# Kernel optimization log

Hardware: AMD Instinct MI355X
Metric: run time of the kernel (lower is better)

The kernel has to match this reference:

```python
import jax, jax.numpy as jnp
import numpy as np

EMB = 512   # emb_dim (== hsz, required by init_decoder feeding enc_sum as hidden)
HSZ = 512   # decoder hidden size
KW, BSZ, PLY = 24, 64, 32  # kw_num, batch, ply_num (decode length = PLY)


def setup_inputs() -> dict:
    key = jax.random.key(0)
    ks = jax.random.split(key, 16)
    s = np.float32(1.0 / np.sqrt(HSZ))
    return {
        "home_col_rep": jax.random.normal(ks[0], (KW, BSZ, PLY, EMB), jnp.float32),
        "home_indices": jax.random.randint(ks[1], (BSZ * KW, PLY), 0, PLY, dtype=jnp.int64),
        "vis_col_rep": jax.random.normal(ks[2], (KW, BSZ, PLY, EMB), jnp.float32),
        "vis_indices": jax.random.randint(ks[3], (BSZ * KW, PLY), 0, PLY, dtype=jnp.int64),
        "team_col_rep": jax.random.normal(ks[4], (KW, BSZ, PLY, EMB), jnp.float32),
        "team_indices": jax.random.randint(ks[5], (BSZ * KW, PLY), 0, PLY, dtype=jnp.int64),
        # learned params
        "init_embed": jax.random.uniform(ks[6], (EMB,), jnp.float32, -1.0, 1.0),
        "W_ih": jax.random.normal(ks[7], (4 * HSZ, EMB), jnp.float32) * s,
        "W_hh": jax.random.normal(ks[8], (4 * HSZ, HSZ), jnp.float32) * s,
        "b_ih": jax.random.normal(ks[9], (4 * HSZ,), jnp.float32) * s,
        "b_hh": jax.random.normal(ks[10], (4 * HSZ,), jnp.float32) * s,
        "Wq": jax.random.normal(ks[11], (HSZ, HSZ), jnp.float32) * s,
        "bq": jax.random.normal(ks[12], (HSZ,), jnp.float32) * s,
        "Wc": jax.random.normal(ks[13], (HSZ, EMB), jnp.float32) * s,
        "v": jax.random.normal(ks[14], (HSZ,), jnp.float32) * s,
    }


def _once(enc4, idx, init_embed, W_ih, W_hh, b_ih, b_hh, Wq, bq, Wc, v):
    kw, bsz, ply, h = enc4.shape
    B = bsz * kw
    # sort_type='col': (kw,bsz,ply,h) -> (bsz,kw,ply,h) -> (B,ply,h)
    enc = jnp.transpose(enc4, (1, 0, 2, 3)).reshape(B, ply, h)
    # gather decoder inputs by indices
    dec_in = jnp.take_along_axis(enc, idx[:, :, None], axis=1)  # (B,ply,h)
    # tgt = [init_embed, dec_in][:-1] -> ply steps
    steps = jnp.concatenate(
        [jnp.broadcast_to(init_embed, (B, 1, h)), dec_in[:, :-1]], axis=1
    )  # (B,ply,h)
    h0 = enc.sum(axis=1)  # (B,h) -> both h and c init (LSTM)
    ctx = jnp.einsum("bpe,he->bph", enc, Wc)  # linear_context, precomputed

    def step(carry, x_t):
        hh, cc = carry
        gates = x_t @ W_ih.T + b_ih + hh @ W_hh.T + b_hh  # (B,4h)
        i, f, g, o = jnp.split(gates, 4, axis=-1)
        cc = jax.nn.sigmoid(f) * cc + jax.nn.sigmoid(i) * jnp.tanh(g)
        hh = jax.nn.sigmoid(o) * jnp.tanh(cc)
        q = hh @ Wq.T + bq                      # linear_query
        sc = jnp.tanh(q[:, None, :] + ctx) @ v  # (B,ply)
        logp = jax.nn.log_softmax(sc, axis=-1)
        return (hh, cc), (logp, jnp.argmax(logp, axis=-1))

    (_, _), (attns, argmaxs) = jax.lax.scan(step, (h0, h0), jnp.transpose(steps, (1, 0, 2)))
    # attns: (ply,B,ply) -> (B,ply,ply); argmaxs: (ply,B) -> (B,ply,1)
    return jnp.transpose(attns, (1, 0, 2)), jnp.transpose(argmaxs)[..., None]


def reference(home_col_rep, home_indices, vis_col_rep, vis_indices,
              team_col_rep, team_indices, init_embed, W_ih, W_hh, b_ih, b_hh,
              Wq, bq, Wc, v):
    p = (init_embed, W_ih, W_hh, b_ih, b_hh, Wq, bq, Wc, v)
    h_att, h_arg = _once(home_col_rep, home_indices, *p)
    v_att, v_arg = _once(vis_col_rep, vis_indices, *p)
    t_att, t_arg = _once(team_col_rep, team_indices, *p)
    return (h_att, v_att, t_att, h_arg, v_arg, t_arg)
```

## Files before the change

### kernel.cpp

```cpp
#include <hip/hip_runtime.h>
#include <hip/hip_bf16.h>
#include <math.h>

#define KW 24
#define BSZn 64
#define PLY 32
#define BROWS 1536
#define RTOT 4608

typedef __attribute__((ext_vector_type(8))) short short8v;
typedef __attribute__((ext_vector_type(4))) float f32x4;

__device__ __forceinline__ float sigmoidf_(float x) { return 1.0f / (1.0f + expf(-x)); }

__device__ __forceinline__ float tanh_fast(float x)
{
    float xc = fminf(fmaxf(x, -40.0f), 40.0f);
    float t = __expf(2.0f * xc);
    return (t - 1.0f) * __builtin_amdgcn_rcpf(t + 1.0f);
}

__device__ __forceinline__ void gload16(const void* g, void* l)
{
    __builtin_amdgcn_global_load_lds(
        (__attribute__((address_space(1))) void*)g,
        (__attribute__((address_space(3))) void*)l, 16, 0, 0);
}

__device__ __forceinline__ void split3(float v, ushort* a, ushort* b, ushort* c)
{
    __hip_bfloat16 h1 = __float2bfloat16(v);  float f1 = __bfloat162float(h1);
    float r1 = v - f1;
    __hip_bfloat16 h2 = __float2bfloat16(r1); float f2 = __bfloat162float(h2);
    float r2 = r1 - f2;
    __hip_bfloat16 h3 = __float2bfloat16(r2);
    *a = *(ushort*)&h1; *b = *(ushort*)&h2; *c = *(ushort*)&h3;
}

__global__ void prep_split(const float* __restrict__ W_ih, const float* __restrict__ W_hh,
                           const float* __restrict__ Wq, const float* __restrict__ Wc,
                           const float* __restrict__ b_ih, const float* __restrict__ b_hh,
                           ushort* __restrict__ Wg0, ushort* __restrict__ Wg1, ushort* __restrict__ Wg2,
                           ushort* __restrict__ Wq0, ushort* __restrict__ Wq1, ushort* __restrict__ Wq2,
                           ushort* __restrict__ Wc0, ushort* __restrict__ Wc1, ushort* __restrict__ Wc2,
                           float* __restrict__ biasG)
{
    int n = blockIdx.x, tid = threadIdx.x;
    if (n < 2048) {
        int ublk = n >> 6, gate = (n >> 4) & 3, ui = n & 15;
        int src = gate * 512 + ublk * 16 + ui;
        for (int k = tid; k < 1024; k += 256) {
            float v = (k < 512) ? W_ih[(size_t)src * 512 + k]
                                : W_hh[(size_t)src * 512 + (k - 512)];
            ushort s0, s1, s2; split3(v, &s0, &s1, &s2);
            Wg0[(size_t)n * 1024 + k] = s0;
            Wg1[(size_t)n * 1024 + k] = s1;
            Wg2[(size_t)n * 1024 + k] = s2;
        }
        if (tid == 0) biasG[src] = b_ih[src] + b_hh[src];
    } else if (n < 2560) {
        int n2 = n - 2048;
        for (int k = tid; k < 512; k += 256) {
            ushort s0, s1, s2; split3(Wq[(size_t)n2 * 512 + k], &s0, &s1, &s2);
            Wq0[(size_t)n2 * 512 + k] = s0;
            Wq1[(size_t)n2 * 512 + k] = s1;
            Wq2[(size_t)n2 * 512 + k] = s2;
        }
    } else {
        int n2 = n - 2560;
        for (int k = tid; k < 512; k += 256) {
            ushort s0, s1, s2; split3(Wc[(size_t)n2 * 512 + k], &s0, &s1, &s2);
            Wc0[(size_t)n2 * 512 + k] = s0;
            Wc1[(size_t)n2 * 512 + k] = s1;
            Wc2[(size_t)n2 * 512 + k] = s2;
        }
    }
}

__global__ void init0(const float* __restrict__ home, const float* __restrict__ vis,
                      const float* __restrict__ team,
                      float* __restrict__ cst, float* __restrict__ hf0)
{
    int row = blockIdx.x, tid = threadIdx.x;
    int tau = row / BROWS, r = row % BROWS;
    const float* enc = (tau == 0) ? home : (tau == 1) ? vis : team;
    const float* base = enc + ((size_t)((r % KW) * BSZn + r / KW) * PLY) * 512;
    for (int e = tid; e < 512; e += 256) {
        float s = 0.0f;
        for (int p = 0; p < PLY; ++p) s += base[(size_t)p * 512 + e];
        size_t o = (size_t)row * 512 + e;
        cst[o] = s;
        hf0[o] = s;
    }
}

__global__ __launch_bounds__(256) void gates_mfma(
    const float* __restrict__ home, const float* __restrict__ vis, const float* __restrict__ team,
    const int* __restrict__ hidx, const int* __restrict__ vidx, const int* __restrict__ tidx,
    const float* __restrict__ init_embed,
    const float* __restrict__ hf_in,
    const ushort* __restrict__ Wg0, const ushort* __restrict__ Wg1, const ushort* __restrict__ Wg2,
    const ushort* __restrict__ Wq0, const ushort* __restrict__ Wq1, const ushort* __restrict__ Wq2,
    const float* __restrict__ biasG, const float* __restrict__ bq,
    float* __restrict__ cst, float* __restrict__ hf_out,
    float* __restrict__ Q4, int bn_off, int qslot, int t)
{
    __shared__ char Lds[49152];
    int tid = threadIdx.x;
    int bm = blockIdx.x, bn = blockIdx.y + bn_off;
    bool isq = bn >= 16;
    int w = tid >> 6, lane = tid & 63;
    int wr = w >> 1, wc = w & 1;
    int r0 = bm * 128;
    int nbase = isq ? (bn - 16) * 128 : bn * 128;
    int ldb = isq ? 512 : 1024;
    int kb0 = isq ? 16 : 0;
    int l4 = lane >> 2, lc = lane & 3;
    int srow = tid >> 1, sh = tid & 1;

    const float* hrow = hf_in + (size_t)(r0 + srow) * 512;
    const float* xrow = init_embed;
    if (!isq && t > 0) {
        int tau = (bm * 128) / BROWS;
        const float* enc = (tau == 0) ? home : (tau == 1) ? vis : team;
        const int* idx = (tau == 0) ? hidx : (tau == 1) ? vidx : tidx;
        int r = r0 + srow - tau * BROWS;
        int j = idx[r * PLY + (t - 1)];
        xrow = enc + ((size_t)((r % KW) * BSZn + r / KW) * PLY + j) * 512;
    }
    const ushort* Bp[3];
    if (isq) { Bp[0] = Wq0; Bp[1] = Wq1; Bp[2] = Wq2; }
    else     { Bp[0] = Wg0; Bp[1] = Wg1; Bp[2] = Wg2; }

    f32x4 acc[4][4];
    #pragma unroll
    for (int i = 0; i < 4; ++i)
        #pragma unroll
        for (int j = 0; j < 4; ++j) acc[i][j] = (f32x4){0.f, 0.f, 0.f, 0.f};

    char* ldsBw = Lds + 24576 + w * 2048;
    char* aw = Lds + srow * 64 + sh * 32;

    for (int kb = kb0; kb < 32; ++kb) {
        int kloc = (kb & 15) * 32;
        const float* src = (!isq && kb < 16) ? xrow : hrow;
        float fv[16];
        *(float4*)&fv[0]  = *(const float4*)(src + kloc + sh * 16);
        *(float4*)&fv[4]  = *(const float4*)(src + kloc + sh * 16 + 4);
        *(float4*)&fv[8]  = *(const float4*)(src + kloc + sh * 16 + 8);
        *(float4*)&fv[12] = *(const float4*)(src + kloc + sh * 16 + 12);
        int bofe = isq ? kloc : kb * 32;
        __syncthreads();
        #pragma unroll
        for (int p = 0; p < 3; ++p) {
            gload16(Bp[p] + (size_t)(nbase + w * 32 + l4) * ldb + bofe + lc * 8,
                    ldsBw + p * 8192);
            gload16(Bp[p] + (size_t)(nbase + w * 32 + 16 + l4) * ldb + bofe + lc * 8,
                    ldsBw + p * 8192 + 1024);
        }
        union { ushort u[16]; uint4 v[2]; } u0, u1, u2;
        #pragma unroll
        for (int j2 = 0; j2 < 16; ++j2) split3(fv[j2], &u0.u[j2], &u1.u[j2], &u2.u[j2]);
        *(uint4*)(aw)              = u0.v[0];
        *(uint4*)(aw + 16)         = u0.v[1];
        *(uint4*)(aw + 8192)       = u1.v[0];
        *(uint4*)(aw + 8192 + 16)  = u1.v[1];
        *(uint4*)(aw + 16384)      = u2.v[0];
        *(uint4*)(aw + 16384 + 16) = u2.v[1];
        __syncthreads();

        #pragma unroll
        for (int a = 0; a < 3; ++a) {
            short8v af[4];
            #pragma unroll
            for (int fm = 0; fm < 4; ++fm)
                af[fm] = *(const short8v*)(Lds + a * 8192 +
                           (wr * 64 + fm * 16 + (lane & 15)) * 64 + (lane >> 4) * 16);
            #pragma unroll
            for (int b = 2; b >= 0; --b) {
                if (a + b > 2) continue;
                const char* LdsB = Lds + 24576 + b * 8192;
                short8v bf[4];
                #pragma unroll
                for (int fn = 0; fn < 4; ++fn)
                    bf[fn] = *(const short8v*)(LdsB +
                               (wc * 64 + fn * 16 + (lane & 15)) * 64 + (lane >> 4) * 16);
                #pragma unroll
                for (int fm = 0; fm < 4; ++fm)
                    #pragma unroll
                    for (int fn = 0; fn < 4; ++fn)
                        acc[fm][fn] = __builtin_amdgcn_mfma_f32_16x16x32_bf16(
                            af[fm], bf[fn], acc[fm][fn], 0, 0, 0);
            }
        }
    }

    if (!isq) {
        int u = (bn * 2 + wc) * 16 + (lane & 15);
        float bI = biasG[u], bF = biasG[512 + u], bG = biasG[1024 + u], bO = biasG[1536 + u];
        #pragma unroll
        for (int fm = 0; fm < 4; ++fm) {
            #pragma unroll
            for (int reg = 0; reg < 4; ++reg) {
                int row = r0 + wr * 64 + fm * 16 + (lane >> 4) * 4 + reg;
                float gi = acc[fm][0][reg] + bI;
                float gf = acc[fm][1][reg] + bF;
                float gg = acc[fm][2][reg] + bG;
                float go = acc[fm][3][reg] + bO;
                size_t ci = (size_t)row * 512 + u;
                float c = cst[ci];
                c = sigmoidf_(gf) * c + sigmoidf_(gi) * tanhf(gg);
                float h = sigmoidf_(go) * tanhf(c);
                cst[ci] = c;
                hf_out[ci] = h;
            }
        }
    } else {
        float* Qout = Q4 + (size_t)qslot * RTOT * 512;
        #pragma unroll
        for (int fn = 0; fn < 4; ++fn) {
            int col = nbase + wc * 64 + fn * 16 + (lane & 15);
            float bqv = bq[col];
            #pragma unroll
            for (int fm = 0; fm < 4; ++fm)
                #pragma unroll
                for (int reg = 0; reg < 4; ++reg) {
                    int row = r0 + wr * 64 + fm * 16 + (lane >> 4) * 4 + reg;
                    Qout[(size_t)row * 512 + col] = acc[fm][fn][reg] + bqv;
                }
        }
    }
}

__global__ __launch_bounds__(256) void ctx_mfma(
    const float* __restrict__ home, const float* __restrict__ vis, const float* __restrict__ team,
    const ushort* __restrict__ Wc0, const ushort* __restrict__ Wc1, const ushort* __restrict__ Wc2,
    float* __restrict__ ctx)
{
    __shared__ char Lds[49152];
    int tid = threadIdx.x;
    int bm = blockIdx.x, bn = blockIdx.y;
    int w = tid >> 6, lane = tid & 63;
    int wr = w >> 1, wc = w & 1;
    int r0 = bm * 128;
    int nbase = bn * 128;
    int l4 = lane >> 2, lc = lane & 3;
    int srow = tid >> 1, sh = tid & 1;

    int R = r0 + srow;
    int tau = r0 / (BROWS * PLY);
    const float* enc = (tau == 0) ? home : (tau == 1) ? vis : team;
    int rr = R % (BROWS * PLY), r = rr >> 5, p = rr & 31;
    const float* arow = enc + ((size_t)((r % KW) * BSZn + r / KW) * PLY + p) * 512;
    const ushort* Bp[3] = {Wc0, Wc1, Wc2};

    f32x4 acc[4][4];
    #pragma unroll
    for (int i = 0; i < 4; ++i)
        #pragma unroll
        for (int j = 0; j < 4; ++j) acc[i][j] = (f32x4){0.f, 0.f, 0.f, 0.f};

    char* ldsBw = Lds + 24576 + w * 2048;
    char* aw = Lds + srow * 64 + sh * 32;

    for (int kb = 0; kb < 16; ++kb) {
        int kloc = kb * 32;
        float fv[16];
        *(float4*)&fv[0]  = *(const float4*)(arow + kloc + sh * 16);
        *(float4*)&fv[4]  = *(const float4*)(arow + kloc + sh * 16 + 4);
        *(float4*)&fv[8]  = *(const float4*)(arow + kloc + sh * 16 + 8);
        *(float4*)&fv[12] = *(const float4*)(arow + kloc + sh * 16 + 12);
        __syncthreads();
        #pragma unroll
        for (int pp = 0; pp < 3; ++pp) {
            gload16(Bp[pp] + (size_t)(nbase + w * 32 + l4) * 512 + kloc + lc * 8,
                    ldsBw + pp * 8192);
            gload16(Bp[pp] + (size_t)(nbase + w * 32 + 16 + l4) * 512 + kloc + lc * 8,
                    ldsBw + pp * 8192 + 1024);
        }
        union { ushort u[16]; uint4 v[2]; } u0, u1, u2;
        #pragma unroll
        for (int j2 = 0; j2 < 16; ++j2) split3(fv[j2], &u0.u[j2], &u1.u[j2], &u2.u[j2]);
        *(uint4*)(aw)              = u0.v[0];
        *(uint4*)(aw + 16)         = u0.v[1];
        *(uint4*)(aw + 8192)       = u1.v[0];
        *(uint4*)(aw + 8192 + 16)  = u1.v[1];
        *(uint4*)(aw + 16384)      = u2.v[0];
        *(uint4*)(aw + 16384 + 16) = u2.v[1];
        __syncthreads();

        #pragma unroll
        for (int a = 0; a < 3; ++a) {
            short8v af[4];
            #pragma unroll
            for (int fm = 0; fm < 4; ++fm)
                af[fm] = *(const short8v*)(Lds + a * 8192 +
                           (wr * 64 + fm * 16 + (lane & 15)) * 64 + (lane >> 4) * 16);
            #pragma unroll
            for (int b = 2; b >= 0; --b) {
                if (a + b > 2) continue;
                const char* LdsB = Lds + 24576 + b * 8192;
                short8v bf[4];
                #pragma unroll
                for (int fn = 0; fn < 4; ++fn)
                    bf[fn] = *(const short8v*)(LdsB +
                               (wc * 64 + fn * 16 + (lane & 15)) * 64 + (lane >> 4) * 16);
                #pragma unroll
                for (int fm = 0; fm < 4; ++fm)
                    #pragma unroll
                    for (int fn = 0; fn < 4; ++fn)
                        acc[fm][fn] = __builtin_amdgcn_mfma_f32_16x16x32_bf16(
                            af[fm], bf[fn], acc[fm][fn], 0, 0, 0);
            }
        }
    }

    #pragma unroll
    for (int fn = 0; fn < 4; ++fn) {
        int col = nbase + wc * 64 + fn * 16 + (lane & 15);
        #pragma unroll
        for (int fm = 0; fm < 4; ++fm)
            #pragma unroll
            for (int reg = 0; reg < 4; ++reg) {
                int row = r0 + wr * 64 + fm * 16 + (lane >> 4) * 4 + reg;
                ctx[(size_t)row * 512 + col] = acc[fm][fn][reg];
            }
    }
}

__global__ __launch_bounds__(256) void attn4r(
    const float* __restrict__ Q4, const float* __restrict__ ctx,
    const float* __restrict__ vvec, float* __restrict__ out, int tbase)
{
    int row = blockIdx.x, tid = threadIdx.x;
    int w = tid >> 6, lane = tid & 63;
    __shared__ float scs[4][PLY];

    float qv[4][8], vv[8];
    #pragma unroll
    for (int s = 0; s < 4; ++s) {
        const float* q = Q4 + ((size_t)s * RTOT + row) * 512 + lane * 8;
        *(float4*)&qv[s][0] = *(const float4*)(q);
        *(float4*)&qv[s][4] = *(const float4*)(q + 4);
    }
    *(float4*)&vv[0] = *(const float4*)(vvec + lane * 8);
    *(float4*)&vv[4] = *(const float4*)(vvec + lane * 8 + 4);
    const float* ctxr = ctx + (size_t)row * PLY * 512 + lane * 8;

    for (int pp = 0; pp < 8; ++pp) {
        int p = w * 8 + pp;
        const float* cp = ctxr + (size_t)p * 512;
        float cv[8];
        *(float4*)&cv[0] = *(const float4*)(cp);
        *(float4*)&cv[4] = *(const float4*)(cp + 4);
        float a[4] = {0.f, 0.f, 0.f, 0.f};
        #pragma unroll
        for (int j = 0; j < 8; ++j) {
            float c = cv[j], ve = vv[j];
            #pragma unroll
            for (int s = 0; s < 4; ++s)
                a[s] += tanh_fast(qv[s][j] + c) * ve;
        }
        #pragma unroll
        for (int off = 1; off < 64; off <<= 1) {
            #pragma unroll
            for (int s = 0; s < 4; ++s) a[s] += __shfl_xor(a[s], off);
        }
        if (lane == 0) {
            #pragma unroll
            for (int s = 0; s < 4; ++s) scs[s][p] = a[s];
        }
    }
    __syncthreads();

    if (tid < 128) {
        int w2 = tid >> 5, l = tid & 31;
        float x = scs[w2][l];
        float bvv = x; int bi = l;
        #pragma unroll
        for (int off = 1; off < 32; off <<= 1) {
            float ov = __shfl_xor(bvv, off, 32);
            int oi = __shfl_xor(bi, off, 32);
            if (ov > bvv || (ov == bvv && oi < bi)) { bvv = ov; bi = oi; }
        }
        float s = expf(x - bvv);
        #pragma unroll
        for (int off = 1; off < 32; off <<= 1) s += __shfl_xor(s, off, 32);
        float lse = logf(s);
        int t = tbase + w2;
        int tau = row / BROWS, r = row % BROWS;
        out[(size_t)tau * (BROWS * 1024) + (size_t)r * 1024 + t * 32 + l] = x - bvv - lse;
        if (l == 0)
            out[(size_t)3 * (BROWS * 1024) + (size_t)tau * (BROWS * 32) + r * 32 + t] = (float)bi;
    }
}

extern "C" void kernel_launch(void* const* d_in, const int* in_sizes, int n_in,
                              void* d_out, int out_size, void* d_ws, size_t ws_size,
                              hipStream_t stream)
{
    const float* home = (const float*)d_in[0];
    const int*   hidx = (const int*)d_in[1];
    const float* vis  = (const float*)d_in[2];
    const int*   vidx = (const int*)d_in[3];
    const float* team = (const float*)d_in[4];
    const int*   tidx = (const int*)d_in[5];
    const float* init_embed = (const float*)d_in[6];
    const float* W_ih = (const float*)d_in[7];
    const float* W_hh = (const float*)d_in[8];
    const float* b_ih = (const float*)d_in[9];
    const float* b_hh = (const float*)d_in[10];
    const float* Wq   = (const float*)d_in[11];
    const float* bq   = (const float*)d_in[12];
    const float* Wc   = (const float*)d_in[13];
    const float* vvec = (const float*)d_in[14];
    float* out = (float*)d_out;
    (void)in_sizes; (void)n_in; (void)out_size; (void)ws_size;

    char* wsb = (char*)d_ws;
    float* ctx   = (float*)wsb; wsb += (size_t)RTOT * PLY * 512 * 4;
    float* cst   = (float*)wsb; wsb += (size_t)RTOT * 512 * 4;
    float* Q4    = (float*)wsb; wsb += (size_t)4 * RTOT * 512 * 4;
    float* biasG = (float*)wsb; wsb += 2048 * 4;
    ushort* Wg[3], *Wq3[3], *Wc3[3];
    for (int i = 0; i < 3; ++i) { Wg[i]  = (ushort*)wsb; wsb += (size_t)2048 * 1024 * 2; }
    for (int i = 0; i < 3; ++i) { Wq3[i] = (ushort*)wsb; wsb += (size_t)512 * 512 * 2; }
    for (int i = 0; i < 3; ++i) { Wc3[i] = (ushort*)wsb; wsb += (size_t)512 * 512 * 2; }
    float* hf[2];
    for (int b = 0; b < 2; ++b) { hf[b] = (float*)wsb; wsb += (size_t)RTOT * 512 * 4; }

    prep_split<<<3072, 256, 0, stream>>>(W_ih, W_hh, Wq, Wc, b_ih, b_hh,
                                         Wg[0], Wg[1], Wg[2], Wq3[0], Wq3[1], Wq3[2],
                                         Wc3[0], Wc3[1], Wc3[2], biasG);
    init0<<<RTOT, 256, 0, stream>>>(home, vis, team, cst, hf[1]);
    ctx_mfma<<<dim3(RTOT * PLY / 128, 4), 256, 0, stream>>>(
        home, vis, team, Wc3[0], Wc3[1], Wc3[2], ctx);

    for (int t = 0; t < 32; ++t) {
        int hin = (t + 1) & 1, hout = t & 1;
        int gy = 16 + ((t >= 1) ? 4 : 0);
        gates_mfma<<<dim3(36, gy), 256, 0, stream>>>(
            home, vis, team, hidx, vidx, tidx, init_embed,
            hf[hin],
            Wg[0], Wg[1], Wg[2], Wq3[0], Wq3[1], Wq3[2],
            biasG, bq, cst, hf[hout],
            Q4, 0, (t - 1) & 3, t);
        if (t >= 4 && (t & 3) == 0)
            attn4r<<<RTOT, 256, 0, stream>>>(Q4, ctx, vvec, out, t - 4);
    }
    gates_mfma<<<dim3(36, 4), 256, 0, stream>>>(
        home, vis, team, hidx, vidx, tidx, init_embed,
        hf[1],
        Wg[0], Wg[1], Wg[2], Wq3[0], Wq3[1], Wq3[2],
        biasG, bq, cst, hf[0],
        Q4, 16, 3, 32);
    attn4r<<<RTOT, 256, 0, stream>>>(Q4, ctx, vvec, out, 28);
}
```

Measured before the change: 6.445 ms.

## Widen gates GEMM N-tile to 256 columns to halve A-tile reloads

The per-step gates/query GEMM kernel now computes a 128x256 output tile per block instead of 128x128. Each wave holds 4x8 accumulators, and the LDS B buffer is doubled, so shared memory grows to 72KB. The goal is to halve redundant loading and bf16 splitting of the A operand (x and h rows) across column blocks, and to launch half as many blocks per step. In exchange, register pressure and LDS use go up, occupancy drops, and the grid shrinks to 36x10 blocks, which may underfill the GPU's CUs.

```diff
diff --git a/kernel.cpp b/kernel.cpp
--- a/kernel.cpp
+++ b/kernel.cpp
@@ -105,14 +105,14 @@
     float* __restrict__ cst, float* __restrict__ hf_out,
     float* __restrict__ Q4, int bn_off, int qslot, int t)
 {
-    __shared__ char Lds[49152];
+    __shared__ char Lds[73728];
     int tid = threadIdx.x;
     int bm = blockIdx.x, bn = blockIdx.y + bn_off;
-    bool isq = bn >= 16;
+    bool isq = bn >= 8;
     int w = tid >> 6, lane = tid & 63;
     int wr = w >> 1, wc = w & 1;
     int r0 = bm * 128;
-    int nbase = isq ? (bn - 16) * 128 : bn * 128;
+    int nbase = isq ? (bn - 8) * 256 : bn * 256;
     int ldb = isq ? 512 : 1024;
     int kb0 = isq ? 16 : 0;
     int l4 = lane >> 2, lc = lane & 3;
@@ -132,13 +132,13 @@
     if (isq) { Bp[0] = Wq0; Bp[1] = Wq1; Bp[2] = Wq2; }
     else     { Bp[0] = Wg0; Bp[1] = Wg1; Bp[2] = Wg2; }
 
-    f32x4 acc[4][4];
+    f32x4 acc[4][8];
     #pragma unroll
     for (int i = 0; i < 4; ++i)
         #pragma unroll
-        for (int j = 0; j < 4; ++j) acc[i][j] = (f32x4){0.f, 0.f, 0.f, 0.f};
-
-    char* ldsBw = Lds + 24576 + w * 2048;
+        for (int j = 0; j < 8; ++j) acc[i][j] = (f32x4){0.f, 0.f, 0.f, 0.f};
+
+    char* ldsBw = Lds + 24576 + w * 4096;
     char* aw = Lds + srow * 64 + sh * 32;
 
     for (int kb = kb0; kb < 32; ++kb) {
@@ -153,10 +153,10 @@
         __syncthreads();
         #pragma unroll
         for (int p = 0; p < 3; ++p) {
-            gload16(Bp[p] + (size_t)(nbase + w * 32 + l4) * ldb + bofe + lc * 8,
-                    ldsBw + p * 8192);
-            gload16(Bp[p] + (size_t)(nbase + w * 32 + 16 + l4) * ldb + bofe + lc * 8,
-                    ldsBw + p * 8192 + 1024);
+            #pragma unroll
+            for (int hh = 0; hh < 4; ++hh)
+                gload16(Bp[p] + (size_t)(nbase + w * 64 + hh * 16 + l4) * ldb + bofe + lc * 8,
+                        ldsBw + p * 16384 + hh * 1024);
         }
         union { ushort u[16]; uint4 v[2]; } u0, u1, u2;
         #pragma unroll
@@ -179,47 +179,49 @@
             #pragma unroll
             for (int b = 2; b >= 0; --b) {
                 if (a + b > 2) continue;
-                const char* LdsB = Lds + 24576 + b * 8192;
-                short8v bf[4];
+                const char* LdsB = Lds + 24576 + b * 16384;
                 #pragma unroll
-                for (int fn = 0; fn < 4; ++fn)
-                    bf[fn] = *(const short8v*)(LdsB +
-                               (wc * 64 + fn * 16 + (lane & 15)) * 64 + (lane >> 4) * 16);
+                for (int fn = 0; fn < 8; ++fn) {
+                    short8v bf = *(const short8v*)(LdsB +
+                               (wc * 128 + fn * 16 + (lane & 15)) * 64 + (lane >> 4) * 16);
+                    #pragma unroll
+                    for (int fm = 0; fm < 4; ++fm)
+                        acc[fm][fn] = __builtin_amdgcn_mfma_f32_16x16x32_bf16(
+                            af[fm], bf, acc[fm][fn], 0, 0, 0);
+                }
+            }
+        }
+    }
+
+    if (!isq) {
+        int u0b = ((nbase >> 6) + wc * 2) * 16 + (lane & 15);
+        #pragma unroll
+        for (int g2 = 0; g2 < 2; ++g2) {
+            int u = u0b + g2 * 16;
+            float bI = biasG[u], bF = biasG[512 + u], bG = biasG[1024 + u], bO = biasG[1536 + u];
+            #pragma unroll
+            for (int fm = 0; fm < 4; ++fm) {
                 #pragma unroll
-                for (int fm = 0; fm < 4; ++fm)
-                    #pragma unroll
-                    for (int fn = 0; fn < 4; ++fn)
-                        acc[fm][fn] = __builtin_amdgcn_mfma_f32_16x16x32_bf16(
-                            af[fm], bf[fn], acc[fm][fn], 0, 0, 0);
-            }
-        }
-    }
-
-    if (!isq) {
-        int u = (bn * 2 + wc) * 16 + (lane & 15);
-        float bI = biasG[u], bF = biasG[512 + u], bG = biasG[1024 + u], bO = biasG[1536 + u];
-        #pragma unroll
-        for (int fm = 0; fm < 4; ++fm) {
-            #pragma unroll
-            for (int reg = 0; reg < 4; ++reg) {
-                int row = r0 + wr * 64 + fm * 16 + (lane >> 4) * 4 + reg;
-                float gi = acc[fm][0][reg] + bI;
-                float gf = acc[fm][1][reg] + bF;
-                float gg = acc[fm][2][reg] + bG;
-                float go = acc[fm][3][reg] + bO;
-                size_t ci = (size_t)row * 512 + u;
-                float c = cst[ci];
-                c = sigmoidf_(gf) * c + sigmoidf_(gi) * tanhf(gg);
-                float h = sigmoidf_(go) * tanhf(c);
-                cst[ci] = c;
-                hf_out[ci] = h;
+                for (int reg = 0; reg < 4; ++reg) {
+                    int row = r0 + wr * 64 + fm * 16 + (lane >> 4) * 4 + reg;
+                    float gi = acc[fm][g2 * 4 + 0][reg] + bI;
+                    float gf = acc[fm][g2 * 4 + 1][reg] + bF;
+                    float gg = acc[fm][g2 * 4 + 2][reg] + bG;
+                    float go = acc[fm][g2 * 4 + 3][reg] + bO;
+                    size_t ci = (size_t)row * 512 + u;
+                    float c = cst[ci];
+                    c = sigmoidf_(gf) * c + sigmoidf_(gi) * tanhf(gg);
+                    float h = sigmoidf_(go) * tanhf(c);
+                    cst[ci] = c;
+                    hf_out[ci] = h;
+                }
             }
         }
     } else {
         float* Qout = Q4 + (size_t)qslot * RTOT * 512;
         #pragma unroll
-        for (int fn = 0; fn < 4; ++fn) {
-            int col = nbase + wc * 64 + fn * 16 + (lane & 15);
+        for (int fn = 0; fn < 8; ++fn) {
+            int col = nbase + wc * 128 + fn * 16 + (lane & 15);
             float bqv = bq[col];
             #pragma unroll
             for (int fm = 0; fm < 4; ++fm)
@@ -438,7 +440,7 @@
 
     for (int t = 0; t < 32; ++t) {
         int hin = (t + 1) & 1, hout = t & 1;
-        int gy = 16 + ((t >= 1) ? 4 : 0);
+        int gy = 8 + ((t >= 1) ? 2 : 0);
         gates_mfma<<<dim3(36, gy), 256, 0, stream>>>(
             home, vis, team, hidx, vidx, tidx, init_embed,
             hf[hin],
@@ -448,11 +450,11 @@
         if (t >= 4 && (t & 3) == 0)
             attn4r<<<RTOT, 256, 0, stream>>>(Q4, ctx, vvec, out, t - 4);
     }
-    gates_mfma<<<dim3(36, 4), 256, 0, stream>>>(
+    gates_mfma<<<dim3(36, 2), 256, 0, stream>>>(
         home, vis, team, hidx, vidx, tidx, init_embed,
         hf[1],
         Wg[0], Wg[1], Wg[2], Wq3[0], Wq3[1], Wq3[2],
         biasG, bq, cst, hf[0],
-        Q4, 16, 3, 32);
+        Q4, 8, 3, 32);
     attn4r<<<RTOT, 256, 0, stream>>>(Q4, ctx, vvec, out, 28);
 }
```

Result: slower. 8.737 ms (+35.6%).
